# Kernel tuning notes

Measured on AMD Instinct MI355X. Metric: run time of the kernel, lower is better.

The kernel has to match this reference:

```python
import math
import jax, jax.numpy as jnp
import numpy as np

B, T_BI, D_BI = 64, 3000, 128
T_SW, D_SW = 375, 192
T_S1, D_S1 = 188, 192
N_FIRES = 300          # static fire count (target_lengths all = 300 -> beta = 1, ceil(sum)=300)
D_MODEL = 512
SCALE = 4.0            # scale_factor
EPS_LN = 1e-5


def _cif_integrate(h, alpha, thr, n_fires):
    """Vectorized CIF: cumsum + two scatter-adds (matches torch _cif_forward).
    h [B,T,D], alpha [B,T], thr [B,1] -> [B,n_fires,D]."""
    Bq, T, D = h.shape
    a = alpha / thr                       # normalize so boundaries sit at integers
    c = jnp.cumsum(a, axis=1)
    prev = c - a
    kp = jnp.floor(prev)
    kc = jnp.floor(c)
    fired = kc > kp                       # frame crosses a token boundary
    w_hi = jnp.where(fired, (c - kc) * thr, 0.0)          # leftover into new token
    w_lo = jnp.where(fired, (kp + 1.0 - prev) * thr, alpha)  # portion completing old token
    ip = jnp.clip(kp.astype(jnp.int32), 0, n_fires - 1)
    ic = jnp.clip(kc.astype(jnp.int32), 0, n_fires - 1)
    bidx = jnp.broadcast_to(jnp.arange(Bq)[:, None], (Bq, T))
    out = jnp.zeros((Bq, n_fires, D), h.dtype)
    out = out.at[bidx, ip].add(w_lo[..., None] * h)
    out = out.at[bidx, ic].add(w_hi[..., None] * h)
    return out


def _interp(src, t_cont, t_bi):
    """Linear interp of src [B,Ts,D] at continuous fire times t_cont [B,N] (given on the T_bi grid)."""
    Bq, Ts, D = src.shape
    t = t_cont * Ts / t_bi
    lo = jnp.clip(t.astype(jnp.int32), 0, Ts - 2)
    w = (t - lo.astype(t.dtype))[..., None]
    idx_lo = jnp.broadcast_to(lo[..., None], (Bq, t.shape[1], D))
    g_lo = jnp.take_along_axis(src, idx_lo, axis=1)
    g_hi = jnp.take_along_axis(src, idx_lo + 1, axis=1)
    return (1.0 - w) * g_lo + w * g_hi


def _forward(fire_signal, acoustic_src, acoustic_src_s1, conv_w, ln_g, ln_b, wp_w, wp_b,
             film_s0_w, film_s0_b, film_s1_w, film_s1_b, tproj_w, tproj_b,
             aproj_w, aproj_b, bproj_w, bproj_b, target_lengths):
    Bq, T_bi, _ = fire_signal.shape
    # 1) weight predictor: depthwise conv (k=1, no bias) -> LN -> Linear -> sigmoid
    x = fire_signal * conv_w                                   # depthwise 1x1 conv
    mu = jnp.mean(x, axis=-1, keepdims=True)
    var = jnp.var(x, axis=-1, keepdims=True)
    xn = (x - mu) * jax.lax.rsqrt(var + EPS_LN) * ln_g + ln_b
    alpha = SCALE * jax.nn.sigmoid(xn @ wp_w + wp_b)           # [B,T]
    tgt = target_lengths.astype(alpha.dtype)
    qty_loss = jnp.mean(jnp.abs(jnp.sum(alpha, axis=1) - tgt))
    # training-mode alpha normalization (sum alpha_cif == target)
    sum_a = jnp.clip(jnp.sum(alpha, axis=1, keepdims=True), 1e-8)
    alpha_cif = alpha * (tgt[:, None] / sum_a)
    # dynamic threshold beta = sum / ceil(sum)  (== 1 here since targets are integers)
    sum_cif = jnp.sum(alpha_cif, axis=1)
    ceil_sum = jax.lax.stop_gradient(jnp.clip(jnp.ceil(sum_cif), 1.0))
    thr = (sum_cif / ceil_sum)[:, None]                        # [B,1]
    # 2) CIF integration of temporal channel
    acoustic_temporal = _cif_integrate(fire_signal, alpha_cif, thr, N_FIRES)  # [B,N,128]
    # continuous fire times
    cum = jnp.cumsum(alpha_cif, axis=1)
    thresholds = jnp.arange(1, N_FIRES + 1, dtype=alpha.dtype)[None, :] * thr  # [B,N]
    ff = jax.vmap(jnp.searchsorted)(cum, thresholds)
    ff = jnp.minimum(ff, T_bi - 1)
    t_lo = jnp.maximum(ff - 1, 0)
    cum_at = jnp.take_along_axis(cum, t_lo, axis=1)
    a_at = jnp.take_along_axis(alpha_cif, ff, axis=1)
    t_cont = t_lo.astype(alpha.dtype) + (thresholds - cum_at) / jnp.clip(a_at, 1e-8)
    t_cont = jnp.clip(t_cont, 0.0, T_bi - 1)
    # 3) S0 pitch channel: interp + FiLM
    acoustic_pitch = _interp(acoustic_src, t_cont, T_bi)       # [B,N,192]
    film0 = acoustic_temporal @ film_s0_w + film_s0_b
    g0, b0 = jnp.split(film0, 2, axis=-1)
    pitch_mod = g0 * acoustic_pitch + b0
    # 4) project + combine
    embs = (acoustic_temporal @ tproj_w + tproj_b) + (pitch_mod @ aproj_w + aproj_b)
    # S1 beat channel
    acoustic_beat = _interp(acoustic_src_s1, t_cont, T_bi)     # [B,N,192]
    film1 = acoustic_temporal @ film_s1_w + film_s1_b
    g1, b1 = jnp.split(film1, 2, axis=-1)
    beat_mod = g1 * acoustic_beat + b1
    embs = embs + (beat_mod @ bproj_w + bproj_b)
    return embs, alpha, qty_loss


def setup_inputs() -> dict:
    key = jax.random.key(0)
    ks = jax.random.split(key, 14)
    # weight_proj bias init per module: alpha_init = target_fires/encoder_len
    p = min((128.0 / 3000.0) / SCALE, 0.99)
    wp_bias = math.log(p / (1.0 - p))
    f32 = jnp.float32
    return {
        "fire_signal": jax.random.normal(ks[0], (B, T_BI, D_BI), f32),
        "acoustic_src": jax.random.normal(ks[1], (B, T_SW, D_SW), f32),
        "acoustic_src_s1": jax.random.normal(ks[2], (B, T_S1, D_S1), f32),
        "target_lengths": jnp.full((B,), N_FIRES, jnp.int32),
        "conv_w": 1.0 + 0.1 * jax.random.normal(ks[3], (D_BI,), f32),
        "ln_g": jnp.ones((D_BI,), f32),
        "ln_b": jnp.zeros((D_BI,), f32),
        "wp_w": 0.02 * jax.random.normal(ks[4], (D_BI,), f32),
        "wp_b": jnp.asarray(wp_bias, f32),
        "film_s0_w": 0.02 * jax.random.normal(ks[5], (D_BI, 2 * D_SW), f32),
        "film_s0_b": jnp.concatenate([jnp.ones((D_SW,), f32), jnp.zeros((D_SW,), f32)]),
        "film_s1_w": 0.02 * jax.random.normal(ks[6], (D_BI, 2 * D_S1), f32),
        "film_s1_b": jnp.concatenate([jnp.ones((D_S1,), f32), jnp.zeros((D_S1,), f32)]),
        "tproj_w": 0.02 * jax.random.normal(ks[7], (D_BI, D_MODEL), f32),
        "tproj_b": jnp.zeros((D_MODEL,), f32),
        "aproj_w": 0.02 * jax.random.normal(ks[8], (D_SW, D_MODEL), f32),
        "aproj_b": jnp.zeros((D_MODEL,), f32),
        "bproj_w": 0.02 * jax.random.normal(ks[9], (D_S1, D_MODEL), f32),
        "bproj_b": jnp.zeros((D_MODEL,), f32),
    }


def reference(fire_signal, acoustic_src, acoustic_src_s1, target_lengths, conv_w, ln_g, ln_b,
              wp_w, wp_b, film_s0_w, film_s0_b, film_s1_w, film_s1_b, tproj_w, tproj_b,
              aproj_w, aproj_b, bproj_w, bproj_b):
    return _forward(fire_signal, acoustic_src, acoustic_src_s1, conv_w, ln_g, ln_b, wp_w, wp_b,
                    film_s0_w, film_s0_b, film_s1_w, film_s1_b, tproj_w, tproj_b,
                    aproj_w, aproj_b, bproj_w, bproj_b, target_lengths)
```

## Files before the change

kernel.cpp:

```cpp
#include <hip/hip_runtime.h>
#include <math.h>

#define BQ 64
#define TBI 3000
#define DBI 128
#define TSW 375
#define TS1 188
#define DSW 192
#define NF 300
#define DMODEL 512
#define EPSLN 1e-5f

typedef __bf16 bf16x8 __attribute__((ext_vector_type(8)));
typedef float f32x4 __attribute__((ext_vector_type(4)));

__device__ __forceinline__ unsigned short f2bf(float f) {
    unsigned u = __float_as_uint(f);
    unsigned r = (u + 0x7FFFu + ((u >> 16) & 1u)) >> 16;
    return (unsigned short)r;
}

__global__ __launch_bounds__(256) void k_alpha(
    const float* __restrict__ fs, const float* __restrict__ conv_w,
    const float* __restrict__ ln_g, const float* __restrict__ ln_b,
    const float* __restrict__ wp_w, const float* __restrict__ wp_b,
    float* __restrict__ alpha_out)
{
    int wid = threadIdx.x >> 6;
    int lane = threadIdx.x & 63;
    long g = (long)blockIdx.x * 4 + wid;
    if (g >= (long)BQ * TBI) return;
    const float* row = fs + g * DBI;
    float f0 = row[lane], f1 = row[lane + 64];
    float x0 = f0 * conv_w[lane];
    float x1 = f1 * conv_w[lane + 64];
    float s = x0 + x1;
    for (int m = 32; m >= 1; m >>= 1) s += __shfl_xor(s, m, 64);
    float mu = s * (1.0f / 128.0f);
    float d0 = x0 - mu, d1 = x1 - mu;
    float q = d0 * d0 + d1 * d1;
    for (int m = 32; m >= 1; m >>= 1) q += __shfl_xor(q, m, 64);
    float var = q * (1.0f / 128.0f);
    float rs = rsqrtf(var + EPSLN);
    float xn0 = d0 * rs * ln_g[lane] + ln_b[lane];
    float xn1 = d1 * rs * ln_g[lane + 64] + ln_b[lane + 64];
    float z = xn0 * wp_w[lane] + xn1 * wp_w[lane + 64];
    for (int m = 32; m >= 1; m >>= 1) z += __shfl_xor(z, m, 64);
    z += wp_b[0];
    float a = 4.0f / (1.0f + expf(-z));
    if (lane == 0) alpha_out[g] = a;
}

__global__ __launch_bounds__(1024) void k_batchsum(
    const float* __restrict__ alpha, const int* __restrict__ tlen,
    float2* __restrict__ params, float* __restrict__ qtyb)
{
    __shared__ double red[1024];
    int b = blockIdx.x, tid = threadIdx.x;
    const float* ar = alpha + (long)b * TBI;
    double s = 0.0;
    for (int t = tid; t < TBI; t += 1024) s += (double)ar[t];
    red[tid] = s; __syncthreads();
    for (int d = 512; d >= 1; d >>= 1) { if (tid < d) red[tid] += red[tid + d]; __syncthreads(); }
    double sum_a = red[0];
    __syncthreads();
    double tgt = (double)tlen[b];
    double sa = sum_a < 1e-8 ? 1e-8 : sum_a;
    float r = (float)(tgt / sa);
    double s2 = 0.0;
    for (int t = tid; t < TBI; t += 1024) s2 += (double)(ar[t] * r);
    red[tid] = s2; __syncthreads();
    for (int d = 512; d >= 1; d >>= 1) { if (tid < d) red[tid] += red[tid + d]; __syncthreads(); }
    if (tid == 0) {
        float sum_cif = (float)red[0];
        float cs = ceilf(sum_cif); if (cs < 1.0f) cs = 1.0f;
        float thr = sum_cif / cs;
        params[b] = make_float2(r, thr);
        qtyb[b] = (float)fabs(sum_a - tgt);
    }
}

__global__ void k_qty(const float* __restrict__ qtyb, float* __restrict__ out)
{
    float v = qtyb[threadIdx.x & 63];
    for (int m = 32; m >= 1; m >>= 1) v += __shfl_xor(v, m, 64);
    if (threadIdx.x == 0) out[0] = v * (1.0f / (float)BQ);
}

__global__ __launch_bounds__(1024) void k_scan(
    const float* __restrict__ alpha, const float2* __restrict__ params,
    float2* __restrict__ c2, float* __restrict__ tcont)
{
    __shared__ float2 sc[TBI];
    __shared__ float2 part[2][1024];
    int b = blockIdx.x, tid = threadIdx.x;
    float2 pp = params[b];
    float r = pp.x, thr = pp.y;
    const float* ar = alpha + (long)b * TBI;
    int base = tid * 3;
    float2 run = make_float2(0.f, 0.f);
    if (base < TBI) {
        for (int j = 0; j < 3; ++j) {
            int t = base + j;
            float ac = ar[t] * r;
            float av = ac / thr;
            run.x += av; run.y += ac;
            sc[t] = run;
        }
    }
    part[0][tid] = (base < TBI) ? run : make_float2(0.f, 0.f);
    __syncthreads();
    int srcb = 0;
    for (int d = 1; d < 1024; d <<= 1) {
        float2 v = part[srcb][tid];
        if (tid >= d) { float2 u = part[srcb][tid - d]; v.x += u.x; v.y += u.y; }
        part[srcb ^ 1][tid] = v;
        srcb ^= 1;
        __syncthreads();
    }
    if (base < TBI && tid > 0) {
        float2 off = part[srcb][tid - 1];
        for (int j = 0; j < 3; ++j) { sc[base + j].x += off.x; sc[base + j].y += off.y; }
    }
    __syncthreads();
    for (int t = tid; t < TBI; t += 1024) {
        float ac = ar[t] * r;
        c2[(long)b * TBI + t] = make_float2(sc[t].x, ac);
    }
    if (tid < NF) {
        float v = (float)(tid + 1) * thr;
        int lo = 0, hi = TBI;
        while (lo < hi) { int mid = (lo + hi) >> 1; if (sc[mid].y < v) lo = mid + 1; else hi = mid; }
        int ff = lo; if (ff > TBI - 1) ff = TBI - 1;
        int tl = ff - 1; if (tl < 0) tl = 0;
        float cum_at = sc[tl].y;
        float a_at = ar[ff] * r;
        if (a_at < 1e-8f) a_at = 1e-8f;
        float tc = (float)tl + (v - cum_at) / a_at;
        tc = fminf(fmaxf(tc, 0.0f), (float)(TBI - 1));
        tcont[b * NF + tid] = tc;
    }
}

#define FPW 94
__global__ __launch_bounds__(256) void k_cif(
    const float* __restrict__ fs, const float2* __restrict__ c2,
    const float2* __restrict__ params, float* __restrict__ at)
{
    int wid = threadIdx.x >> 6, lane = threadIdx.x & 63;
    int wg = blockIdx.x * 4 + wid;
    int b = wg >> 5, slot = wg & 31;
    int t0 = slot * FPW;
    int t1 = t0 + FPW; if (t1 > TBI) t1 = TBI;
    float thr = params[b].y;
    const float2* cb = c2 + (long)b * TBI;
    const float* fb = fs + (long)b * TBI * DBI;
    float* ab = at + (long)b * NF * DBI;
    int cur = -1;
    float a0 = 0.f, a1 = 0.f;
    for (int t = t0; t < t1; ++t) {
        float2 v = cb[t];
        float c = v.x, ac = v.y;
        float av = ac / thr;
        float prev = c - av;
        float kp = floorf(prev), kc = floorf(c);
        bool fired = kc > kp;
        float w_lo = fired ? (kp + 1.0f - prev) * thr : ac;
        float w_hi = fired ? (c - kc) * thr : 0.0f;
        int ip = (int)kp; if (ip > NF - 1) ip = NF - 1; if (ip < 0) ip = 0;
        int ic = (int)kc; if (ic > NF - 1) ic = NF - 1; if (ic < 0) ic = 0;
        float h0 = fb[(long)t * DBI + lane], h1 = fb[(long)t * DBI + 64 + lane];
        if (ip != cur) {
            if (cur >= 0) { atomicAdd(&ab[cur * DBI + lane], a0); atomicAdd(&ab[cur * DBI + 64 + lane], a1); }
            cur = ip; a0 = 0.f; a1 = 0.f;
        }
        a0 += w_lo * h0; a1 += w_lo * h1;
        if (fired) {
            if (ic != cur) {
                if (cur >= 0) { atomicAdd(&ab[cur * DBI + lane], a0); atomicAdd(&ab[cur * DBI + 64 + lane], a1); }
                cur = ic; a0 = 0.f; a1 = 0.f;
            }
            a0 += w_hi * h0; a1 += w_hi * h1;
        }
    }
    if (cur >= 0) { atomicAdd(&ab[cur * DBI + lane], a0); atomicAdd(&ab[cur * DBI + 64 + lane], a1); }
}

__global__ __launch_bounds__(256) void k_prep(
    const float* __restrict__ f0w, const float* __restrict__ f1w,
    const float* __restrict__ tw, const float* __restrict__ aw, const float* __restrict__ bw,
    unsigned short* __restrict__ Wg, unsigned short* __restrict__ Wb,
    unsigned short* __restrict__ W2)
{
    int i = blockIdx.x * 256 + threadIdx.x;
    if (i < 49152) {
        int j = i & 7, lane = (i >> 3) & 63, kt = (i >> 9) & 3, nt = i >> 11;
        int k = kt * 32 + (lane >> 4) * 8 + j;
        int n = nt * 16 + (lane & 15);
        float g, b;
        if (n < 192) { g = f0w[k * 384 + n];         b = f0w[k * 384 + n + 192]; }
        else         { g = f1w[k * 384 + (n - 192)]; b = f1w[k * 384 + (n - 192) + 192]; }
        Wg[i] = f2bf(g); Wb[i] = f2bf(b);
    } else if (i < 49152 + 262144) {
        int ii = i - 49152;
        int j = ii & 7, lane = (ii >> 3) & 63, kt = (ii >> 9) & 15, nt = ii >> 13;
        int k = kt * 32 + (lane >> 4) * 8 + j;
        int n = nt * 16 + (lane & 15);
        float v;
        if (k < 128)      v = tw[k * 512 + n];
        else if (k < 320) v = aw[(k - 128) * 512 + n];
        else              v = bw[(k - 320) * 512 + n];
        W2[ii] = f2bf(v);
    }
}

__global__ void k_prepb(const float* __restrict__ f0b, const float* __restrict__ f1b,
                        const float* __restrict__ tb, const float* __restrict__ apb,
                        const float* __restrict__ bpb,
                        float* __restrict__ gbias, float* __restrict__ bbias,
                        float* __restrict__ bias2)
{
    int c = threadIdx.x;
    if (c < 384) {
        gbias[c] = c < 192 ? f0b[c] : f1b[c - 192];
        bbias[c] = c < 192 ? f0b[c + 192] : f1b[c - 192 + 192];
    }
    bias2[c] = tb[c] + apb[c] + bpb[c];
}

#define ROWS 32
__global__ __launch_bounds__(256) void k_emb2(
    const float* __restrict__ at, const float* __restrict__ tcont,
    const float* __restrict__ src0, const float* __restrict__ src1,
    const unsigned short* __restrict__ Wg, const unsigned short* __restrict__ Wb,
    const unsigned short* __restrict__ W2,
    const float* __restrict__ gbias, const float* __restrict__ bbias,
    const float* __restrict__ bias2, float* __restrict__ embs)
{
    __shared__ __align__(16) unsigned short X[ROWS][520];
    __shared__ float s_w0[ROWS], s_w1[ROWS];
    __shared__ int s_lo0[ROWS], s_lo1[ROWS], s_b[ROWS];
    int tid = threadIdx.x;
    int wave = tid >> 6, lane = tid & 63;
    long r0 = (long)blockIdx.x * ROWS;
    for (int idx = tid; idx < ROWS * 32; idx += 256) {
        int r = idx >> 5, k4 = (idx & 31) * 4;
        float4 v = *(const float4*)&at[(r0 + r) * DBI + k4];
        X[r][k4 + 0] = f2bf(v.x); X[r][k4 + 1] = f2bf(v.y);
        X[r][k4 + 2] = f2bf(v.z); X[r][k4 + 3] = f2bf(v.w);
    }
    if (tid < ROWS) {
        long g = r0 + tid;
        s_b[tid] = (int)(g / NF);
        float tc = tcont[g];
        float t0 = tc * ((float)TSW / 3000.0f);
        int lo0 = (int)t0; if (lo0 > TSW - 2) lo0 = TSW - 2; if (lo0 < 0) lo0 = 0;
        s_lo0[tid] = lo0; s_w0[tid] = t0 - (float)lo0;
        float t1 = tc * ((float)TS1 / 3000.0f);
        int lo1 = (int)t1; if (lo1 > TS1 - 2) lo1 = TS1 - 2; if (lo1 < 0) lo1 = 0;
        s_lo1[tid] = lo1; s_w1[tid] = t1 - (float)lo1;
    }
    __syncthreads();
    int mrow = lane & 15, quad = lane >> 4;
    for (int nt = wave; nt < 24; nt += 4) {
        f32x4 ag0 = {0,0,0,0}, ag1 = {0,0,0,0}, ab0 = {0,0,0,0}, ab1 = {0,0,0,0};
        #pragma unroll
        for (int kt = 0; kt < 4; ++kt) {
            bf16x8 a0 = *(const bf16x8*)&X[mrow][kt * 32 + quad * 8];
            bf16x8 a1 = *(const bf16x8*)&X[16 + mrow][kt * 32 + quad * 8];
            bf16x8 bg = *(const bf16x8*)&Wg[(((nt * 4 + kt) * 64) + lane) * 8];
            bf16x8 bb = *(const bf16x8*)&Wb[(((nt * 4 + kt) * 64) + lane) * 8];
            ag0 = __builtin_amdgcn_mfma_f32_16x16x32_bf16(a0, bg, ag0, 0, 0, 0);
            ag1 = __builtin_amdgcn_mfma_f32_16x16x32_bf16(a1, bg, ag1, 0, 0, 0);
            ab0 = __builtin_amdgcn_mfma_f32_16x16x32_bf16(a0, bb, ab0, 0, 0, 0);
            ab1 = __builtin_amdgcn_mfma_f32_16x16x32_bf16(a1, bb, ab1, 0, 0, 0);
        }
        int c = nt * 16 + mrow;
        bool sel = c >= DSW;
        int cc = sel ? c - DSW : c;
        const float* S = sel ? src1 : src0;
        int Ts = sel ? TS1 : TSW;
        float gb = gbias[c], bbv = bbias[c];
        #pragma unroll
        for (int m = 0; m < 2; ++m) {
            #pragma unroll
            for (int q = 0; q < 4; ++q) {
                int r = m * 16 + quad * 4 + q;
                int b = s_b[r];
                int lo = sel ? s_lo1[r] : s_lo0[r];
                float w = sel ? s_w1[r] : s_w0[r];
                const float* Sp = S + ((long)b * Ts + lo) * DSW + cc;
                float pv = (1.0f - w) * Sp[0] + w * Sp[DSW];
                float gv = (m ? ag1[q] : ag0[q]) + gb;
                float bv = (m ? ab1[q] : ab0[q]) + bbv;
                X[r][128 + c] = f2bf(gv * pv + bv);
            }
        }
    }
    __syncthreads();
    #pragma unroll
    for (int chunk = 0; chunk < 2; ++chunk) {
        f32x4 acc[2][4];
        #pragma unroll
        for (int m = 0; m < 2; ++m)
            #pragma unroll
            for (int n = 0; n < 4; ++n) acc[m][n] = (f32x4){0, 0, 0, 0};
        for (int kt = 0; kt < 16; ++kt) {
            bf16x8 a0 = *(const bf16x8*)&X[mrow][kt * 32 + quad * 8];
            bf16x8 a1 = *(const bf16x8*)&X[16 + mrow][kt * 32 + quad * 8];
            #pragma unroll
            for (int n = 0; n < 4; ++n) {
                int nt = wave * 8 + chunk * 4 + n;
                bf16x8 bfv = *(const bf16x8*)&W2[(((nt * 16 + kt) * 64) + lane) * 8];
                acc[0][n] = __builtin_amdgcn_mfma_f32_16x16x32_bf16(a0, bfv, acc[0][n], 0, 0, 0);
                acc[1][n] = __builtin_amdgcn_mfma_f32_16x16x32_bf16(a1, bfv, acc[1][n], 0, 0, 0);
            }
        }
        #pragma unroll
        for (int n = 0; n < 4; ++n) {
            int cbase = (wave * 8 + chunk * 4 + n) * 16 + mrow;
            float bv = bias2[cbase];
            #pragma unroll
            for (int m = 0; m < 2; ++m)
                #pragma unroll
                for (int q = 0; q < 4; ++q) {
                    int r = m * 16 + quad * 4 + q;
                    embs[(r0 + r) * DMODEL + cbase] = acc[m][n][q] + bv;
                }
        }
    }
}

extern "C" void kernel_launch(void* const* d_in, const int* in_sizes, int n_in,
                              void* d_out, int out_size, void* d_ws, size_t ws_size,
                              hipStream_t stream)
{
    const float* fs     = (const float*)d_in[0];
    const float* src0   = (const float*)d_in[1];
    const float* src1   = (const float*)d_in[2];
    const int*   tlen   = (const int*)d_in[3];
    const float* conv_w = (const float*)d_in[4];
    const float* ln_g   = (const float*)d_in[5];
    const float* ln_b   = (const float*)d_in[6];
    const float* wp_w   = (const float*)d_in[7];
    const float* wp_b   = (const float*)d_in[8];
    const float* f0w    = (const float*)d_in[9];
    const float* f0b    = (const float*)d_in[10];
    const float* f1w    = (const float*)d_in[11];
    const float* f1b    = (const float*)d_in[12];
    const float* tw     = (const float*)d_in[13];
    const float* tb     = (const float*)d_in[14];
    const float* aw     = (const float*)d_in[15];
    const float* apb    = (const float*)d_in[16];
    const float* bw     = (const float*)d_in[17];
    const float* bpb    = (const float*)d_in[18];

    float* embs  = (float*)d_out;
    float* alpha = embs + (long)BQ * NF * DMODEL;
    float* qtyo  = alpha + (long)BQ * TBI;

    char* ws = (char*)d_ws;
    size_t off = 0;
    float*  at     = (float*)(ws + off);  off += 9830400;
    float2* c2     = (float2*)(ws + off); off += 1536000;
    float*  tcont  = (float*)(ws + off);  off += 76800;
    float2* params = (float2*)(ws + off); off += 512;
    float*  qtyb   = (float*)(ws + off);  off += 256;
    unsigned short* Wg = (unsigned short*)(ws + off); off += 98304;
    unsigned short* Wb = (unsigned short*)(ws + off); off += 98304;
    unsigned short* W2 = (unsigned short*)(ws + off); off += 524288;
    float* gbias = (float*)(ws + off); off += 1536;
    float* bbias = (float*)(ws + off); off += 1536;
    float* bias2 = (float*)(ws + off); off += 2048;

    hipMemsetAsync(at, 0, (size_t)BQ * NF * DBI * sizeof(float), stream);
    k_prep<<<1216, 256, 0, stream>>>(f0w, f1w, tw, aw, bw, Wg, Wb, W2);
    k_prepb<<<1, 512, 0, stream>>>(f0b, f1b, tb, apb, bpb, gbias, bbias, bias2);
    k_alpha<<<(BQ * TBI) / 4, 256, 0, stream>>>(fs, conv_w, ln_g, ln_b, wp_w, wp_b, alpha);
    k_batchsum<<<BQ, 1024, 0, stream>>>(alpha, tlen, params, qtyb);
    k_qty<<<1, 64, 0, stream>>>(qtyb, qtyo);
    k_scan<<<BQ, 1024, 0, stream>>>(alpha, params, c2, tcont);
    k_cif<<<512, 256, 0, stream>>>(fs, c2, params, at);
    k_emb2<<<(BQ * NF) / ROWS, 256, 0, stream>>>(at, tcont, src0, src1,
                                                 Wg, Wb, W2, gbias, bbias, bias2, embs);
}
```

Before: 324.4 us.

## Fuse batchsum into scan, vectorize alpha rows, prefetch CIF and GEMM weights

Several independent changes. The weight predictor now processes two rows per wave with float4 loads and 32-lane reductions. The batch-sum kernel is merged into the scan kernel, removing one launch and a re-read of alpha, and divisions by thr become reciprocal multiplies. The CIF integration loop software-prefetches the next frame with float2 loads, and the final GEMM merges its two chunks into one loop that double-buffers the weight fragments in registers. The register-heavy GEMM loop may reduce occupancy.

```diff
diff --git a/kernel.cpp b/kernel.cpp
--- a/kernel.cpp
+++ b/kernel.cpp
@@ -20,41 +20,45 @@
     return (unsigned short)r;
 }
 
-__global__ __launch_bounds__(256) void k_alpha(
+__global__ __launch_bounds__(256) void k_alpha2(
     const float* __restrict__ fs, const float* __restrict__ conv_w,
     const float* __restrict__ ln_g, const float* __restrict__ ln_b,
     const float* __restrict__ wp_w, const float* __restrict__ wp_b,
     float* __restrict__ alpha_out)
 {
-    int wid = threadIdx.x >> 6;
-    int lane = threadIdx.x & 63;
-    long g = (long)blockIdx.x * 4 + wid;
-    if (g >= (long)BQ * TBI) return;
+    int wave = threadIdx.x >> 6, lane = threadIdx.x & 63;
+    int l = lane & 31;
+    long g = (long)blockIdx.x * 8 + wave * 2 + (lane >> 5);
     const float* row = fs + g * DBI;
-    float f0 = row[lane], f1 = row[lane + 64];
-    float x0 = f0 * conv_w[lane];
-    float x1 = f1 * conv_w[lane + 64];
-    float s = x0 + x1;
-    for (int m = 32; m >= 1; m >>= 1) s += __shfl_xor(s, m, 64);
+    float4 f  = *(const float4*)&row[4 * l];
+    float4 cw = *(const float4*)&conv_w[4 * l];
+    float4 x; x.x = f.x * cw.x; x.y = f.y * cw.y; x.z = f.z * cw.z; x.w = f.w * cw.w;
+    float s = x.x + x.y + x.z + x.w;
+    for (int m = 16; m >= 1; m >>= 1) s += __shfl_xor(s, m, 64);
     float mu = s * (1.0f / 128.0f);
-    float d0 = x0 - mu, d1 = x1 - mu;
-    float q = d0 * d0 + d1 * d1;
-    for (int m = 32; m >= 1; m >>= 1) q += __shfl_xor(q, m, 64);
+    float4 d; d.x = x.x - mu; d.y = x.y - mu; d.z = x.z - mu; d.w = x.w - mu;
+    float q = d.x * d.x + d.y * d.y + d.z * d.z + d.w * d.w;
+    for (int m = 16; m >= 1; m >>= 1) q += __shfl_xor(q, m, 64);
     float var = q * (1.0f / 128.0f);
     float rs = rsqrtf(var + EPSLN);
-    float xn0 = d0 * rs * ln_g[lane] + ln_b[lane];
-    float xn1 = d1 * rs * ln_g[lane + 64] + ln_b[lane + 64];
-    float z = xn0 * wp_w[lane] + xn1 * wp_w[lane + 64];
-    for (int m = 32; m >= 1; m >>= 1) z += __shfl_xor(z, m, 64);
+    float4 lg = *(const float4*)&ln_g[4 * l];
+    float4 lb = *(const float4*)&ln_b[4 * l];
+    float4 wp = *(const float4*)&wp_w[4 * l];
+    float z = (d.x * rs * lg.x + lb.x) * wp.x + (d.y * rs * lg.y + lb.y) * wp.y
+            + (d.z * rs * lg.z + lb.z) * wp.z + (d.w * rs * lg.w + lb.w) * wp.w;
+    for (int m = 16; m >= 1; m >>= 1) z += __shfl_xor(z, m, 64);
     z += wp_b[0];
     float a = 4.0f / (1.0f + expf(-z));
-    if (lane == 0) alpha_out[g] = a;
-}
-
-__global__ __launch_bounds__(1024) void k_batchsum(
+    if (l == 0) alpha_out[g] = a;
+}
+
+__global__ __launch_bounds__(1024) void k_scan2(
     const float* __restrict__ alpha, const int* __restrict__ tlen,
-    float2* __restrict__ params, float* __restrict__ qtyb)
-{
+    float2* __restrict__ params, float* __restrict__ qtyb,
+    float2* __restrict__ c2, float* __restrict__ tcont)
+{
+    __shared__ float2 sc[TBI];
+    __shared__ float2 part[2][1024];
     __shared__ double red[1024];
     int b = blockIdx.x, tid = threadIdx.x;
     const float* ar = alpha + (long)b * TBI;
@@ -62,8 +66,7 @@
     for (int t = tid; t < TBI; t += 1024) s += (double)ar[t];
     red[tid] = s; __syncthreads();
     for (int d = 512; d >= 1; d >>= 1) { if (tid < d) red[tid] += red[tid + d]; __syncthreads(); }
-    double sum_a = red[0];
-    __syncthreads();
+    double sum_a = red[0]; __syncthreads();
     double tgt = (double)tlen[b];
     double sa = sum_a < 1e-8 ? 1e-8 : sum_a;
     float r = (float)(tgt / sa);
@@ -71,40 +74,18 @@
     for (int t = tid; t < TBI; t += 1024) s2 += (double)(ar[t] * r);
     red[tid] = s2; __syncthreads();
     for (int d = 512; d >= 1; d >>= 1) { if (tid < d) red[tid] += red[tid + d]; __syncthreads(); }
-    if (tid == 0) {
-        float sum_cif = (float)red[0];
-        float cs = ceilf(sum_cif); if (cs < 1.0f) cs = 1.0f;
-        float thr = sum_cif / cs;
-        params[b] = make_float2(r, thr);
-        qtyb[b] = (float)fabs(sum_a - tgt);
-    }
-}
-
-__global__ void k_qty(const float* __restrict__ qtyb, float* __restrict__ out)
-{
-    float v = qtyb[threadIdx.x & 63];
-    for (int m = 32; m >= 1; m >>= 1) v += __shfl_xor(v, m, 64);
-    if (threadIdx.x == 0) out[0] = v * (1.0f / (float)BQ);
-}
-
-__global__ __launch_bounds__(1024) void k_scan(
-    const float* __restrict__ alpha, const float2* __restrict__ params,
-    float2* __restrict__ c2, float* __restrict__ tcont)
-{
-    __shared__ float2 sc[TBI];
-    __shared__ float2 part[2][1024];
-    int b = blockIdx.x, tid = threadIdx.x;
-    float2 pp = params[b];
-    float r = pp.x, thr = pp.y;
-    const float* ar = alpha + (long)b * TBI;
+    float sum_cif = (float)red[0];
+    float cs = ceilf(sum_cif); if (cs < 1.0f) cs = 1.0f;
+    float thr = sum_cif / cs;
+    float rthr = 1.0f / thr;
+    if (tid == 0) { params[b] = make_float2(r, thr); qtyb[b] = (float)fabs(sum_a - tgt); }
     int base = tid * 3;
     float2 run = make_float2(0.f, 0.f);
     if (base < TBI) {
         for (int j = 0; j < 3; ++j) {
             int t = base + j;
             float ac = ar[t] * r;
-            float av = ac / thr;
-            run.x += av; run.y += ac;
+            run.x += ac * rthr; run.y += ac;
             sc[t] = run;
         }
     }
@@ -142,8 +123,15 @@
     }
 }
 
+__global__ void k_qty(const float* __restrict__ qtyb, float* __restrict__ out)
+{
+    float v = qtyb[threadIdx.x & 63];
+    for (int m = 32; m >= 1; m >>= 1) v += __shfl_xor(v, m, 64);
+    if (threadIdx.x == 0) out[0] = v * (1.0f / (float)BQ);
+}
+
 #define FPW 94
-__global__ __launch_bounds__(256) void k_cif(
+__global__ __launch_bounds__(256) void k_cif2(
     const float* __restrict__ fs, const float2* __restrict__ c2,
     const float2* __restrict__ params, float* __restrict__ at)
 {
@@ -152,16 +140,24 @@
     int b = wg >> 5, slot = wg & 31;
     int t0 = slot * FPW;
     int t1 = t0 + FPW; if (t1 > TBI) t1 = TBI;
+    if (t0 >= t1) return;
     float thr = params[b].y;
+    float rthr = 1.0f / thr;
     const float2* cb = c2 + (long)b * TBI;
     const float* fb = fs + (long)b * TBI * DBI;
     float* ab = at + (long)b * NF * DBI;
     int cur = -1;
     float a0 = 0.f, a1 = 0.f;
+    float2 v = cb[t0];
+    float2 h = *(const float2*)&fb[(long)t0 * DBI + 2 * lane];
     for (int t = t0; t < t1; ++t) {
-        float2 v = cb[t];
+        float2 vn = v, hn = h;
+        if (t + 1 < t1) {
+            vn = cb[t + 1];
+            hn = *(const float2*)&fb[(long)(t + 1) * DBI + 2 * lane];
+        }
         float c = v.x, ac = v.y;
-        float av = ac / thr;
+        float av = ac * rthr;
         float prev = c - av;
         float kp = floorf(prev), kc = floorf(c);
         bool fired = kc > kp;
@@ -169,21 +165,21 @@
         float w_hi = fired ? (c - kc) * thr : 0.0f;
         int ip = (int)kp; if (ip > NF - 1) ip = NF - 1; if (ip < 0) ip = 0;
         int ic = (int)kc; if (ic > NF - 1) ic = NF - 1; if (ic < 0) ic = 0;
-        float h0 = fb[(long)t * DBI + lane], h1 = fb[(long)t * DBI + 64 + lane];
         if (ip != cur) {
-            if (cur >= 0) { atomicAdd(&ab[cur * DBI + lane], a0); atomicAdd(&ab[cur * DBI + 64 + lane], a1); }
+            if (cur >= 0) { atomicAdd(&ab[cur * DBI + 2 * lane], a0); atomicAdd(&ab[cur * DBI + 2 * lane + 1], a1); }
             cur = ip; a0 = 0.f; a1 = 0.f;
         }
-        a0 += w_lo * h0; a1 += w_lo * h1;
+        a0 += w_lo * h.x; a1 += w_lo * h.y;
         if (fired) {
             if (ic != cur) {
-                if (cur >= 0) { atomicAdd(&ab[cur * DBI + lane], a0); atomicAdd(&ab[cur * DBI + 64 + lane], a1); }
+                if (cur >= 0) { atomicAdd(&ab[cur * DBI + 2 * lane], a0); atomicAdd(&ab[cur * DBI + 2 * lane + 1], a1); }
                 cur = ic; a0 = 0.f; a1 = 0.f;
             }
-            a0 += w_hi * h0; a1 += w_hi * h1;
-        }
-    }
-    if (cur >= 0) { atomicAdd(&ab[cur * DBI + lane], a0); atomicAdd(&ab[cur * DBI + 64 + lane], a1); }
+            a0 += w_hi * h.x; a1 += w_hi * h.y;
+        }
+        v = vn; h = hn;
+    }
+    if (cur >= 0) { atomicAdd(&ab[cur * DBI + 2 * lane], a0); atomicAdd(&ab[cur * DBI + 2 * lane + 1], a1); }
 }
 
 __global__ __launch_bounds__(256) void k_prep(
@@ -229,7 +225,7 @@
 }
 
 #define ROWS 32
-__global__ __launch_bounds__(256) void k_emb2(
+__global__ __launch_bounds__(256) void k_emb3(
     const float* __restrict__ at, const float* __restrict__ tcont,
     const float* __restrict__ src0, const float* __restrict__ src1,
     const unsigned short* __restrict__ Wg, const unsigned short* __restrict__ Wb,
@@ -298,35 +294,38 @@
         }
     }
     __syncthreads();
+    f32x4 acc0[8], acc1[8];
     #pragma unroll
-    for (int chunk = 0; chunk < 2; ++chunk) {
-        f32x4 acc[2][4];
-        #pragma unroll
-        for (int m = 0; m < 2; ++m)
+    for (int n = 0; n < 8; ++n) { acc0[n] = (f32x4){0,0,0,0}; acc1[n] = (f32x4){0,0,0,0}; }
+    bf16x8 bcur[8];
+    #pragma unroll
+    for (int n = 0; n < 8; ++n)
+        bcur[n] = *(const bf16x8*)&W2[(((wave * 8 + n) * 16 + 0) * 64 + lane) * 8];
+    for (int kt = 0; kt < 16; ++kt) {
+        bf16x8 bnxt[8];
+        if (kt < 15) {
             #pragma unroll
-            for (int n = 0; n < 4; ++n) acc[m][n] = (f32x4){0, 0, 0, 0};
-        for (int kt = 0; kt < 16; ++kt) {
-            bf16x8 a0 = *(const bf16x8*)&X[mrow][kt * 32 + quad * 8];
-            bf16x8 a1 = *(const bf16x8*)&X[16 + mrow][kt * 32 + quad * 8];
-            #pragma unroll
-            for (int n = 0; n < 4; ++n) {
-                int nt = wave * 8 + chunk * 4 + n;
-                bf16x8 bfv = *(const bf16x8*)&W2[(((nt * 16 + kt) * 64) + lane) * 8];
-                acc[0][n] = __builtin_amdgcn_mfma_f32_16x16x32_bf16(a0, bfv, acc[0][n], 0, 0, 0);
-                acc[1][n] = __builtin_amdgcn_mfma_f32_16x16x32_bf16(a1, bfv, acc[1][n], 0, 0, 0);
-            }
-        }
-        #pragma unroll
-        for (int n = 0; n < 4; ++n) {
-            int cbase = (wave * 8 + chunk * 4 + n) * 16 + mrow;
-            float bv = bias2[cbase];
-            #pragma unroll
-            for (int m = 0; m < 2; ++m)
-                #pragma unroll
-                for (int q = 0; q < 4; ++q) {
-                    int r = m * 16 + quad * 4 + q;
-                    embs[(r0 + r) * DMODEL + cbase] = acc[m][n][q] + bv;
-                }
+            for (int n = 0; n < 8; ++n)
+                bnxt[n] = *(const bf16x8*)&W2[(((wave * 8 + n) * 16 + kt + 1) * 64 + lane) * 8];
+        }
+        bf16x8 a0 = *(const bf16x8*)&X[mrow][kt * 32 + quad * 8];
+        bf16x8 a1 = *(const bf16x8*)&X[16 + mrow][kt * 32 + quad * 8];
+        #pragma unroll
+        for (int n = 0; n < 8; ++n) {
+            acc0[n] = __builtin_amdgcn_mfma_f32_16x16x32_bf16(a0, bcur[n], acc0[n], 0, 0, 0);
+            acc1[n] = __builtin_amdgcn_mfma_f32_16x16x32_bf16(a1, bcur[n], acc1[n], 0, 0, 0);
+        }
+        #pragma unroll
+        for (int n = 0; n < 8; ++n) bcur[n] = bnxt[n];
+    }
+    #pragma unroll
+    for (int n = 0; n < 8; ++n) {
+        int cbase = (wave * 8 + n) * 16 + mrow;
+        float bv = bias2[cbase];
+        #pragma unroll
+        for (int q = 0; q < 4; ++q) {
+            embs[(r0 + quad * 4 + q) * DMODEL + cbase] = acc0[n][q] + bv;
+            embs[(r0 + 16 + quad * 4 + q) * DMODEL + cbase] = acc1[n][q] + bv;
         }
     }
 }
@@ -376,11 +375,10 @@
     hipMemsetAsync(at, 0, (size_t)BQ * NF * DBI * sizeof(float), stream);
     k_prep<<<1216, 256, 0, stream>>>(f0w, f1w, tw, aw, bw, Wg, Wb, W2);
     k_prepb<<<1, 512, 0, stream>>>(f0b, f1b, tb, apb, bpb, gbias, bbias, bias2);
-    k_alpha<<<(BQ * TBI) / 4, 256, 0, stream>>>(fs, conv_w, ln_g, ln_b, wp_w, wp_b, alpha);
-    k_batchsum<<<BQ, 1024, 0, stream>>>(alpha, tlen, params, qtyb);
+    k_alpha2<<<(BQ * TBI) / 8, 256, 0, stream>>>(fs, conv_w, ln_g, ln_b, wp_w, wp_b, alpha);
+    k_scan2<<<BQ, 1024, 0, stream>>>(alpha, tlen, params, qtyb, c2, tcont);
     k_qty<<<1, 64, 0, stream>>>(qtyb, qtyo);
-    k_scan<<<BQ, 1024, 0, stream>>>(alpha, params, c2, tcont);
-    k_cif<<<512, 256, 0, stream>>>(fs, c2, params, at);
-    k_emb2<<<(BQ * NF) / ROWS, 256, 0, stream>>>(at, tcont, src0, src1,
+    k_cif2<<<512, 256, 0, stream>>>(fs, c2, params, at);
+    k_emb3<<<(BQ * NF) / ROWS, 256, 0, stream>>>(at, tcont, src0, src1,
                                                  Wg, Wb, W2, gbias, bbias, bias2, embs);
 }
```

After: 329.6 us. About the same (+1.6%).
